# Kernel tuning notes

Measured on AMD Instinct MI355X. Metric: run time of the kernel, lower is better.

## Reference

```python
import jax, jax.numpy as jnp
import numpy as np

B, S, D_MODEL = 2, 2048, 768
N_QK, D_QK = 16, 16
N_OV, D_OV = 256, 1
VKV = 16
ROT_DIM, ROT_BASE = 16, 10000.0
SCALE = D_QK ** 0.5  # attn_scale defaults to sqrt(d_qk_head)


def _rotary_sin_cos(n_ctx, rotary_dim, base):
    # TransformerLens-style, non-adjacent pairs (GPT-NeoX)
    pos = jnp.arange(n_ctx, dtype=jnp.float32)
    dim = jnp.arange(rotary_dim // 2, dtype=jnp.float32)
    freq = base ** (dim / (rotary_dim / 2))
    freq = jnp.concatenate([freq, freq])  # 'd -> (2 d)'
    angles = pos[:, None] / freq[None, :]  # [n_ctx, rotary_dim]
    return jnp.sin(angles), jnp.cos(angles)


def _apply_rotary(x, sin, cos):
    # x: [B, S, H, d_head]; rotate first ROT_DIM dims, pass through the rest
    s = x.shape[1]
    xr = x[..., :ROT_DIM]
    half = ROT_DIM // 2
    rot = jnp.concatenate([-xr[..., half:], xr[..., :half]], axis=-1)  # rotate_every_two (non-adjacent)
    xr = xr * cos[:s, None, :] + rot * sin[:s, None, :]
    return jnp.concatenate([xr, x[..., ROT_DIM:]], axis=-1) if x.shape[-1] > ROT_DIM else xr


def setup_inputs() -> dict:
    key = jax.random.key(0)
    ks = jax.random.split(key, 6)
    std_qk = np.sqrt(2.0 / (D_MODEL * D_QK))   # kaiming fan_in for [H, d_model, d_head]
    std_v = np.sqrt(2.0 / (D_MODEL * D_OV))
    std_o = np.sqrt(2.0 / (D_OV * D_MODEL))
    std_vk = np.sqrt(2.0 / (N_QK * D_QK))
    return {
        "resid": jax.random.normal(ks[0], (B, S, D_MODEL), jnp.float32),
        "W_Q": jax.random.normal(ks[1], (N_QK, D_MODEL, D_QK), jnp.float32) * std_qk,
        "W_K": jax.random.normal(ks[2], (N_QK, D_MODEL, D_QK), jnp.float32) * std_qk,
        "W_V": jax.random.normal(ks[3], (N_OV, D_MODEL, D_OV), jnp.float32) * std_v,
        "W_O": jax.random.normal(ks[4], (N_OV, D_OV, D_MODEL), jnp.float32) * std_o,
        "b_Q": jnp.zeros((N_QK, D_QK), jnp.float32),
        "b_K": jnp.zeros((N_QK, D_QK), jnp.float32),
        "b_V": jnp.zeros((N_OV, D_OV), jnp.float32),
        "b_O": jnp.zeros((D_MODEL,), jnp.float32),
        "virtual_k": jax.random.normal(ks[5], (VKV, N_QK, D_QK), jnp.float32) * std_vk,
        "virtual_v": jnp.zeros((VKV, N_OV, D_OV), jnp.float32),
    }


def reference(resid, W_Q, W_K, W_V, W_O, b_Q, b_K, b_V, b_O, virtual_k, virtual_v):
    b, s, _ = resid.shape
    sin, cos = _rotary_sin_cos(s, ROT_DIM, ROT_BASE)

    q = jnp.einsum('bsd,hde->bshe', resid, W_Q) + b_Q  # [B,S,N_QK,D_QK]
    k = jnp.einsum('bsd,hde->bshe', resid, W_K) + b_K
    v = jnp.einsum('bsd,hde->bshe', resid, W_V) + b_V  # [B,S,N_OV,1]

    q = _apply_rotary(q, sin, cos)
    k = _apply_rotary(k, sin, cos)

    # append virtual KV along key axis
    k = jnp.concatenate([k, jnp.broadcast_to(virtual_k[None], (b, VKV, N_QK, D_QK))], axis=1)
    v = jnp.concatenate([v, jnp.broadcast_to(virtual_v[None], (b, VKV, N_OV, D_OV))], axis=1)

    scores = jnp.einsum('bqhe,bkhe->bhqk', q, k) / SCALE  # [B,H,S,S+VKV]
    i = jnp.arange(s)[:, None]
    j = jnp.arange(s + VKV)[None, :]
    mask = (j - i) <= VKV  # tril(.., diagonal=VKV)
    scores = jnp.where(mask, scores, -jnp.inf)
    pattern = jax.nn.softmax(scores, axis=-1)
    pattern = jnp.where(jnp.isnan(pattern), 0.0, pattern)

    r = N_OV // N_QK
    v_r = v.transpose(0, 2, 1, 3).reshape(b, N_QK, r, s + VKV, D_OV)  # [B,n_qk,r,K,1]
    z = jnp.einsum('bnqk,bnrkh->bnrqh', pattern, v_r)  # [B,n_qk,r,S,1]
    z = z.reshape(b, N_OV, s, D_OV).transpose(0, 2, 1, 3)  # [B,S,N_OV,1]

    out = jnp.einsum('bqhd,hdm->bqm', z, W_O) + b_O  # [B,S,D_MODEL]
    return out
```

## Files before the change

### kernel.cpp

```cpp
#include <hip/hip_runtime.h>
#include <hip/hip_bf16.h>
#include <math.h>

#define B_   2
#define S_   2048
#define DM   768
#define H_   16
#define C_   256
#define VKV_ 16
#define SK   2064
#define SKP  2080
#define NT_  65

#define TSPLIT 16
#define MAXSP  5
#define NACT   164

typedef __attribute__((ext_vector_type(8))) short short8;
typedef __attribute__((ext_vector_type(4))) short short4v;
typedef __attribute__((ext_vector_type(4))) float f32x4;
typedef __attribute__((ext_vector_type(16))) float f32x16;
typedef __attribute__((ext_vector_type(4))) unsigned uint4v;

#define QSCALE 0.360673760222240851f
#define L2B8   1.6609640474436811f

__device__ __forceinline__ short tobf(float f) {
    union { float f; unsigned u; } x; x.f = f;
    unsigned r = x.u + 0x7FFFu + ((x.u >> 16) & 1u);
    return (short)(r >> 16);
}
__device__ __forceinline__ float frombf_lo(unsigned u) {
    union { unsigned u; float f; } x; x.u = u << 16; return x.f;
}
__device__ __forceinline__ float frombf_hi(unsigned u) {
    union { unsigned u; float f; } x; x.u = u & 0xFFFF0000u; return x.f;
}

__device__ __forceinline__ void gload_lds16(const short* g, short* l) {
    __builtin_amdgcn_global_load_lds(
        (const __attribute__((address_space(1))) unsigned int*)g,
        (__attribute__((address_space(3))) unsigned int*)l, 16, 0, 0);
}

#define NRES (4096*768/4)
#define NWQ  (768*768)
#define NWO  (768*256)
__global__ __launch_bounds__(256) void conv_all(
    const float* __restrict__ resid,
    const float* __restrict__ WQ, const float* __restrict__ WK,
    const float* __restrict__ WV, const float* __restrict__ WO,
    const float* __restrict__ bQ, const float* __restrict__ bK,
    const float* __restrict__ bV,
    const float* __restrict__ vKp, const float* __restrict__ vVp,
    short* __restrict__ Ab, short* __restrict__ Wqkv_t,
    short* __restrict__ WtO, float* __restrict__ bqkv,
    short* __restrict__ Kb2, short* __restrict__ Vt3)
{
    int t = blockIdx.x * 256 + threadIdx.x;
    if (t < NRES) {
        float4 v = *(const float4*)(resid + (size_t)t * 4);
        short4v o = { tobf(v.x), tobf(v.y), tobf(v.z), tobf(v.w) };
        *(short4v*)(Ab + (size_t)t * 4) = o;
        return;
    }
    t -= NRES;
    if (t < NWQ) {
        int cc = t / 768, d = t % 768;
        float w;
        if (cc < 256)      w = WQ[((size_t)(cc >> 4) * DM + d) * 16 + (cc & 15)];
        else if (cc < 512) w = WK[((size_t)((cc - 256) >> 4) * DM + d) * 16 + (cc & 15)];
        else               w = WV[(size_t)(cc - 512) * DM + d];
        Wqkv_t[t] = tobf(w);
        return;
    }
    t -= NWQ;
    if (t < NWO) {
        int c = t & 255, m = t >> 8;
        WtO[t] = tobf(WO[(size_t)c * DM + m]);
        return;
    }
    t -= NWO;
    if (t < 768) {
        bqkv[t] = (t < 256) ? bQ[t] : (t < 512 ? bK[t - 256] : bV[t - 512]);
        return;
    }
    t -= 768;
    if (t < 32 * 32) {
        const int bh = t >> 5;
        const int s  = S_ + (t & 31);
        const int h  = bh & 15;
        short kb[16], vb[16];
        if (s < SK) {
            const int tt = s - S_;
#pragma unroll
            for (int e = 0; e < 16; ++e) {
                kb[e] = tobf(vKp[(size_t)tt * 256 + h * 16 + e]);
                vb[e] = tobf(vVp[(size_t)tt * 256 + h * 16 + e]);
            }
        } else {
#pragma unroll
            for (int e = 0; e < 16; ++e) { kb[e] = 0; vb[e] = 0; }
        }
        const int t5 = s >> 5;
        short* kbase = Kb2 + ((size_t)bh * NT_ + t5) * 512 + (s & 31) * 8;
#pragma unroll
        for (int e = 0; e < 8; ++e)  { kbase[e] = kb[e]; kbase[256 + e] = kb[e + 8]; }
        short* vbase = Vt3 + ((size_t)bh * NT_ + t5) * 1024
                     + ((s >> 4) & 1) * 512 + ((s >> 3) & 1) * 8 + (s & 7);
#pragma unroll
        for (int dv = 0; dv < 16; ++dv) vbase[dv * 16] = vb[dv];
    }
}

__global__ __launch_bounds__(256) void mm_qkv(
    const short* __restrict__ A, const short* __restrict__ Bt,
    const float* __restrict__ bias,
    short* __restrict__ Qb2, short* __restrict__ Kb2, short* __restrict__ Vt3)
{
    __shared__ short As[128 * 64];
    __shared__ short Bs[64 * 64];

    const int tid  = threadIdx.x;
    const int w    = tid >> 6;
    const int lane = tid & 63;
    const int wm   = w >> 1, wn = w & 1;
    const int g    = lane >> 4, c = lane & 15;

    const int linear = blockIdx.y * 12 + blockIdx.x;
    const int xcd  = linear & 7;
    const int jj2  = linear >> 3;
    const int m0   = (xcd * 4 + jj2 / 12) * 128;
    const int n0   = (jj2 % 12) * 64;

    f32x4 acc[4][2];
#pragma unroll
    for (int i = 0; i < 4; ++i)
#pragma unroll
        for (int j = 0; j < 2; ++j) acc[i][j] = (f32x4){0.f, 0.f, 0.f, 0.f};

    const int lr = lane >> 3;
    const int lc = lane & 7;

    for (int k0 = 0; k0 < 768; k0 += 64) {
#pragma unroll
        for (int i = 0; i < 4; ++i) {
            const int ch  = i * 4 + w;
            const int row = ch * 8 + lr;
            const int scc = lc ^ (row & 7);
            gload_lds16(A + (size_t)(m0 + row) * 768 + k0 + scc * 8, As + ch * 512);
        }
#pragma unroll
        for (int i = 0; i < 2; ++i) {
            const int ch  = i * 4 + w;
            const int row = ch * 8 + lr;
            const int scc = lc ^ (row & 7);
            gload_lds16(Bt + (size_t)(n0 + row) * 768 + k0 + scc * 8, Bs + ch * 512);
        }
        __syncthreads();
#pragma unroll
        for (int kk = 0; kk < 64; kk += 32) {
            short8 af[4], bf[2];
#pragma unroll
            for (int i = 0; i < 4; ++i) {
                const int row = wm * 64 + i * 16 + c;
                const int sc  = ((kk >> 3) + g) ^ (row & 7);
                af[i] = *(const short8*)(As + row * 64 + sc * 8);
            }
#pragma unroll
            for (int j = 0; j < 2; ++j) {
                const int row = wn * 32 + j * 16 + c;
                const int sc  = ((kk >> 3) + g) ^ (row & 7);
                bf[j] = *(const short8*)(Bs + row * 64 + sc * 8);
            }
#pragma unroll
            for (int i = 0; i < 4; ++i)
#pragma unroll
                for (int j = 0; j < 2; ++j)
                    acc[i][j] = __builtin_amdgcn_mfma_f32_16x16x32_bf16(
                        af[i], bf[j], acc[i][j], 0, 0, 0);
        }
        __syncthreads();
    }

    const float bv0 = bias[n0 + wn * 32 + c];
    const float bv1 = bias[n0 + wn * 32 + 16 + c];

    if (n0 < 512) {
        const int isQ = (n0 < 256) ? 1 : 0;
        const float invf = __builtin_amdgcn_exp2f(-(float)(c & 7) * L2B8);
        const int h0 = (((n0 + wn * 32) & 255) >> 4);
        const int elo = (c & 8) ? 0 : 1;
#pragma unroll
        for (int i = 0; i < 4; ++i) {
#pragma unroll
            for (int r = 0; r < 4; ++r) {
                const int row = m0 + wm * 64 + i * 16 + 4 * g + r;
                const int s   = row & 2047;
                const int b   = row >> 11;
                float sn, cs;
                __sincosf((float)s * invf, &sn, &cs);
#pragma unroll
                for (int j = 0; j < 2; ++j) {
                    float val = acc[i][j][r] + (j ? bv1 : bv0);
                    float par = __shfl_xor(val, 8);
                    float rot = elo ? -par : par;
                    float out = val * cs + rot * sn;
                    if (isQ) out *= QSCALE;
                    const int bh = b * 16 + h0 + j;
                    const size_t base = isQ
                        ? ((size_t)bh * 64 + (s >> 5)) * 512
                        : ((size_t)bh * NT_ + (s >> 5)) * 512;
                    short* dst = (isQ ? Qb2 : Kb2) + base
                               + (s & 31) * 8 + (c >> 3) * 256 + (c & 7);
                    *dst = tobf(out);
                }
            }
        }
    } else {
        const int h0 = ((n0 + wn * 32 - 512) >> 4);
#pragma unroll
        for (int i = 0; i < 4; ++i) {
#pragma unroll
            for (int r = 0; r < 4; ++r) {
                const int row = m0 + wm * 64 + i * 16 + 4 * g + r;
                const int s   = row & 2047;
                const int b   = row >> 11;
#pragma unroll
                for (int j = 0; j < 2; ++j) {
                    float val = acc[i][j][r] + (j ? bv1 : bv0);
                    const int bh = b * 16 + h0 + j;
                    short* dst = Vt3 + ((size_t)bh * NT_ + (s >> 5)) * 1024
                               + ((s >> 4) & 1) * 512 + ((s >> 3) & 1) * 8 + (s & 7)
                               + c * 16;
                    *dst = tobf(val);
                }
            }
        }
    }
}

__global__ __launch_bounds__(256) void mm_out(
    const short* __restrict__ A, const short* __restrict__ Bt,
    const float* __restrict__ bias, float* __restrict__ Cout)
{
    __shared__ short As[128 * 64];
    __shared__ short Bs[64 * 64];

    const int tid  = threadIdx.x;
    const int w    = tid >> 6;
    const int lane = tid & 63;
    const int wm   = w >> 1, wn = w & 1;
    const int g    = lane >> 4, c = lane & 15;

    const int linear = blockIdx.y * 12 + blockIdx.x;
    const int xcd  = linear & 7;
    const int jj2  = linear >> 3;
    const int m0   = (xcd * 4 + jj2 / 12) * 128;
    const int n0   = (jj2 % 12) * 64;

    f32x4 acc[4][2];
#pragma unroll
    for (int i = 0; i < 4; ++i)
#pragma unroll
        for (int j = 0; j < 2; ++j) acc[i][j] = (f32x4){0.f, 0.f, 0.f, 0.f};

    const int lr = lane >> 3;
    const int lc = lane & 7;

    for (int k0 = 0; k0 < 256; k0 += 64) {
#pragma unroll
        for (int i = 0; i < 4; ++i) {
            const int ch  = i * 4 + w;
            const int row = ch * 8 + lr;
            const int scc = lc ^ (row & 7);
            gload_lds16(A + (size_t)(m0 + row) * 256 + k0 + scc * 8, As + ch * 512);
        }
#pragma unroll
        for (int i = 0; i < 2; ++i) {
            const int ch  = i * 4 + w;
            const int row = ch * 8 + lr;
            const int scc = lc ^ (row & 7);
            gload_lds16(Bt + (size_t)(n0 + row) * 256 + k0 + scc * 8, Bs + ch * 512);
        }
        __syncthreads();
#pragma unroll
        for (int kk = 0; kk < 64; kk += 32) {
            short8 af[4], bf[2];
#pragma unroll
            for (int i = 0; i < 4; ++i) {
                const int row = wm * 64 + i * 16 + c;
                const int sc  = ((kk >> 3) + g) ^ (row & 7);
                af[i] = *(const short8*)(As + row * 64 + sc * 8);
            }
#pragma unroll
            for (int j = 0; j < 2; ++j) {
                const int row = wn * 32 + j * 16 + c;
                const int sc  = ((kk >> 3) + g) ^ (row & 7);
                bf[j] = *(const short8*)(Bs + row * 64 + sc * 8);
            }
#pragma unroll
            for (int i = 0; i < 4; ++i)
#pragma unroll
                for (int j = 0; j < 2; ++j)
                    acc[i][j] = __builtin_amdgcn_mfma_f32_16x16x32_bf16(
                        af[i], bf[j], acc[i][j], 0, 0, 0);
        }
        __syncthreads();
    }
#pragma unroll
    for (int i = 0; i < 4; ++i)
#pragma unroll
        for (int j = 0; j < 2; ++j) {
            const int col = n0 + wn * 32 + j * 16 + c;
            const float bv = bias[col];
#pragma unroll
            for (int r = 0; r < 4; ++r) {
                const int row = m0 + wm * 64 + i * 16 + 4 * g + r;
                Cout[(size_t)row * DM + col] = acc[i][j][r] + bv;
            }
        }
}

__global__ __launch_bounds__(256) void attn_split(
    const short* __restrict__ Qb2, const short* __restrict__ Kb2,
    const short* __restrict__ Vt3, unsigned* __restrict__ PartA,
    float* __restrict__ PartL)
{
    const int w    = threadIdx.x >> 6;
    const int lane = threadIdx.x & 63;
    const int blk  = blockIdx.x;
    const int xcd  = blk & 7;
    const int j    = blk >> 3;
    const int bhl  = j / 41;
    const int slot = j - bhl * 41;
    const int bh   = xcd * 4 + bhl;
    const int r    = slot * 4 + w;
    int qt, sp;
    if (r < 49)       { sp = 1; qt = 15 + r; }
    else if (r < 82)  { sp = 2; qt = 31 + (r - 49); }
    else if (r < 99)  { sp = 3; qt = 47 + (r - 82); }
    else if (r == 99) { sp = 4; qt = 63; }
    else              { sp = 0; qt = 163 - r; }

    const int nt   = qt + 2;
    const int t0   = sp * TSPLIT;
    const int tend = min(t0 + TSPLIT, nt);

    const int hi = lane >> 5;
    const int qc = lane & 31;
    const int q0 = qt * 32;

    const f32x16 zero16 = {0,0,0,0,0,0,0,0,0,0,0,0,0,0,0,0};

    short8 qf = *(const short8*)(Qb2 + ((size_t)bh * 64 + qt) * 512 + lane * 8);

    f32x16 acc = zero16;
    float lsum = 0.f;

    const short* kbase = Kb2 + (size_t)bh * NT_ * 512 + lane * 8;
    const short* vbase = Vt3 + (size_t)bh * NT_ * 1024 + (lane & 15) * 16 + hi * 8;
    const int qv16  = q0 + qc + 16;
    const int tmask = (q0 + 17) >> 5;

#define LK(tt)  (*(const short8*)(kbase + (size_t)(tt) * 512))
#define LVA(tt) (*(const short8*)(vbase + (size_t)(tt) * 1024))
#define LVB(tt) (*(const short8*)(vbase + (size_t)(tt) * 1024 + 512))

#define SOFTMAX_TILE(S, tt, B1, B2)                                          \
    {                                                                        \
        if ((tt) >= tmask) {                                                 \
            const int kt_ = (tt) * 32;                                       \
            _Pragma("unroll")                                                \
            for (int rr = 0; rr < 16; ++rr) {                                \
                const int key = kt_ + (rr & 3) + 8 * (rr >> 2) + 4 * hi;     \
                S[rr] = (key <= qv16) ? S[rr] : -INFINITY;                   \
            }                                                                \
        }                                                                    \
        unsigned pk[8];                                                      \
        _Pragma("unroll")                                                    \
        for (int jj = 0; jj < 8; ++jj) {                                     \
            const float p0 = __builtin_amdgcn_exp2f(S[2 * jj]);              \
            const float p1 = __builtin_amdgcn_exp2f(S[2 * jj + 1]);          \
            lsum += p0 + p1;                                                 \
            asm("v_cvt_pk_bf16_f32 %0, %1, %2" : "=v"(pk[jj]) : "v"(p0), "v"(p1)); \
        }                                                                    \
        unsigned a0 = pk[0], a2 = pk[2], a1 = pk[1], a3 = pk[3];             \
        unsigned a4 = pk[4], a6 = pk[6], a5 = pk[5], a7 = pk[7];             \
        asm("v_permlane32_swap_b32 %0, %1" : "+v"(a0), "+v"(a2));            \
        asm("v_permlane32_swap_b32 %0, %1" : "+v"(a1), "+v"(a3));            \
        asm("v_permlane32_swap_b32 %0, %1" : "+v"(a4), "+v"(a6));            \
        asm("v_permlane32_swap_b32 %0, %1" : "+v"(a5), "+v"(a7));            \
        B1.u[0] = a0; B1.u[1] = a1; B1.u[2] = a2; B1.u[3] = a3;              \
        B2.u[0] = a4; B2.u[1] = a5; B2.u[2] = a6; B2.u[3] = a7;              \
    }

    const int npair_end = t0 + ((tend - t0) & ~1);

    if (t0 < npair_end) {
        short8 kfA = LK(t0),     vaA = LVA(t0),     vvA = LVB(t0);
        short8 kfB = LK(t0 + 1), vaB = LVA(t0 + 1), vvB = LVB(t0 + 1);

        for (int t = t0; t < npair_end; t += 2) {
            short8 kfA_n = kfA, vaA_n = vaA, vvA_n = vvA;
            short8 kfB_n = kfB, vaB_n = vaB, vvB_n = vvB;
            if (t + 2 < npair_end) {
                kfA_n = LK(t + 2); vaA_n = LVA(t + 2); vvA_n = LVB(t + 2);
                kfB_n = LK(t + 3); vaB_n = LVA(t + 3); vvB_n = LVB(t + 3);
            }

            __builtin_amdgcn_s_setprio(1);
            f32x16 S0 = __builtin_amdgcn_mfma_f32_32x32x16_bf16(kfA, qf, zero16, 0, 0, 0);
            f32x16 S1 = __builtin_amdgcn_mfma_f32_32x32x16_bf16(kfB, qf, zero16, 0, 0, 0);
            __builtin_amdgcn_s_setprio(0);

            union { unsigned u[4]; short8 v; } b1A, b2A, b1B, b2B;
            SOFTMAX_TILE(S0, t,     b1A, b2A);
            SOFTMAX_TILE(S1, t + 1, b1B, b2B);

            __builtin_amdgcn_s_setprio(1);
            acc = __builtin_amdgcn_mfma_f32_32x32x16_bf16(vaA, b1A.v, acc, 0, 0, 0);
            acc = __builtin_amdgcn_mfma_f32_32x32x16_bf16(vvA, b2A.v, acc, 0, 0, 0);
            acc = __builtin_amdgcn_mfma_f32_32x32x16_bf16(vaB, b1B.v, acc, 0, 0, 0);
            acc = __builtin_amdgcn_mfma_f32_32x32x16_bf16(vvB, b2B.v, acc, 0, 0, 0);
            __builtin_amdgcn_s_setprio(0);

            kfA = kfA_n; vaA = vaA_n; vvA = vvA_n;
            kfB = kfB_n; vaB = vaB_n; vvB = vvB_n;
        }
    }
    if (npair_end < tend) {
        const int t = npair_end;
        short8 kf = LK(t), va = LVA(t), vv = LVB(t);
        f32x16 S0 = __builtin_amdgcn_mfma_f32_32x32x16_bf16(kf, qf, zero16, 0, 0, 0);
        union { unsigned u[4]; short8 v; } b1, b2;
        SOFTMAX_TILE(S0, t, b1, b2);
        acc = __builtin_amdgcn_mfma_f32_32x32x16_bf16(va, b1.v, acc, 0, 0, 0);
        acc = __builtin_amdgcn_mfma_f32_32x32x16_bf16(vv, b2.v, acc, 0, 0, 0);
    }

    uint4v pa;
    asm("v_cvt_pk_bf16_f32 %0, %1, %2" : "=v"(pa.x) : "v"(acc[0]), "v"(acc[1]));
    asm("v_cvt_pk_bf16_f32 %0, %1, %2" : "=v"(pa.y) : "v"(acc[2]), "v"(acc[3]));
    asm("v_cvt_pk_bf16_f32 %0, %1, %2" : "=v"(pa.z) : "v"(acc[4]), "v"(acc[5]));
    asm("v_cvt_pk_bf16_f32 %0, %1, %2" : "=v"(pa.w) : "v"(acc[6]), "v"(acc[7]));

    const int pidx = (bh * 64 + qt) * MAXSP + sp;
    *(uint4v*)(PartA + ((size_t)pidx * 64 + lane) * 4) = pa;

    lsum += __shfl_xor(lsum, 32);
    if (hi == 0) PartL[(size_t)pidx * 32 + qc] = lsum;
}

__global__ __launch_bounds__(256) void attn_combine(
    const unsigned* __restrict__ PartA, const float* __restrict__ PartL,
    short* __restrict__ Zb)
{
    const int w    = threadIdx.x >> 6;
    const int lane = threadIdx.x & 63;
    const int wid  = blockIdx.x * 4 + w;
    const int bh   = wid >> 6;
    const int qt   = wid & 63;
    const int hi   = lane >> 5;
    const int qc   = lane & 31;
    const int ns   = (qt + 2 + TSPLIT - 1) / TSPLIT;

    float a[8];
#pragma unroll
    for (int rr = 0; rr < 8; ++rr) a[rr] = 0.f;
    float lsum = 0.f;

    const int pbase = (bh * 64 + qt) * MAXSP;
    for (int sp = 0; sp < ns; ++sp) {
        uint4v pa = *(const uint4v*)(PartA + ((size_t)(pbase + sp) * 64 + lane) * 4);
        a[0] += frombf_lo(pa.x); a[1] += frombf_hi(pa.x);
        a[2] += frombf_lo(pa.y); a[3] += frombf_hi(pa.y);
        a[4] += frombf_lo(pa.z); a[5] += frombf_hi(pa.z);
        a[6] += frombf_lo(pa.w); a[7] += frombf_hi(pa.w);
        lsum += PartL[(size_t)(pbase + sp) * 32 + qc];
    }
    const float inv = 1.f / lsum;

    const int b = bh >> 4, h = bh & 15;
    const int q0 = qt * 32;
    short* zp = Zb + ((size_t)(b * S_ + q0 + qc)) * C_ + h * 16;
    unsigned o01, o23, o45, o67;
    {
        float a0 = a[0] * inv, a1 = a[1] * inv, a2 = a[2] * inv, a3 = a[3] * inv;
        float a4 = a[4] * inv, a5 = a[5] * inv, a6 = a[6] * inv, a7 = a[7] * inv;
        asm("v_cvt_pk_bf16_f32 %0, %1, %2" : "=v"(o01) : "v"(a0), "v"(a1));
        asm("v_cvt_pk_bf16_f32 %0, %1, %2" : "=v"(o23) : "v"(a2), "v"(a3));
        asm("v_cvt_pk_bf16_f32 %0, %1, %2" : "=v"(o45) : "v"(a4), "v"(a5));
        asm("v_cvt_pk_bf16_f32 %0, %1, %2" : "=v"(o67) : "v"(a6), "v"(a7));
    }
    *(unsigned*)(zp + 4 * hi)         = o01;
    *(unsigned*)(zp + 4 * hi + 2)     = o23;
    *(unsigned*)(zp + 8 + 4 * hi)     = o45;
    *(unsigned*)(zp + 8 + 4 * hi + 2) = o67;
}

extern "C" void kernel_launch(void* const* d_in, const int* in_sizes, int n_in,
                              void* d_out, int out_size, void* d_ws, size_t ws_size,
                              hipStream_t stream)
{
    const float* resid = (const float*)d_in[0];
    const float* WQ = (const float*)d_in[1];
    const float* WK = (const float*)d_in[2];
    const float* WV = (const float*)d_in[3];
    const float* WO = (const float*)d_in[4];
    const float* bQ = (const float*)d_in[5];
    const float* bK = (const float*)d_in[6];
    const float* bV = (const float*)d_in[7];
    const float* bO = (const float*)d_in[8];
    const float* vK = (const float*)d_in[9];
    const float* vV = (const float*)d_in[10];
    float* out = (float*)d_out;
    float* ws  = (float*)d_ws;

    short* Zb   = (short*)ws;
    float* bqkv = ws + 3145728;
    short* Ab   = (short*)(ws + 3145728 + 768);
    short* Wqt  = Ab + 3145728;
    short* WtO  = Wqt + 589824;
    short* Qb2  = WtO + 196608;
    short* Kb2  = Qb2 + 1048576;
    short* Vt3  = Kb2 + 1064960;
    unsigned* PartA = (unsigned*)(Vt3 + 2129920);
    float*    PartL = (float*)(PartA + 2621440);

    const int conv_total = NRES + NWQ + NWO + 768 + 1024;
    conv_all<<<dim3((conv_total + 255) / 256), 256, 0, stream>>>(
        resid, WQ, WK, WV, WO, bQ, bK, bV, vK, vV,
        Ab, Wqt, WtO, bqkv, Kb2, Vt3);
    mm_qkv<<<dim3(12, 32), 256, 0, stream>>>(Ab, Wqt, bqkv, Qb2, Kb2, Vt3);
    attn_split<<<dim3(32 * NACT / 4), 256, 0, stream>>>(Qb2, Kb2, Vt3, PartA, PartL);
    attn_combine<<<dim3(512), 256, 0, stream>>>(PartA, PartL, Zb);
    mm_out<<<dim3(12, 32), 256, 0, stream>>>(Zb, WtO, bO, out);
}
```

Before: 60.02 us.

## Double-buffer LDS tiles in QKV and output GEMMs to overlap loads with MFMA

Both GEMM kernels now keep two LDS buffers for the A and B tiles. Each iteration first issues the direct-to-LDS loads for the next K tile, then runs MFMAs on the current tile, so global-memory latency can hide behind compute and one barrier per iteration goes away. In exchange, shared memory per block doubles, which may lower how many blocks fit on a CU. These GEMMs are only part of a pipeline that attention likely dominates.

```diff
diff --git a/kernel.cpp b/kernel.cpp
--- a/kernel.cpp
+++ b/kernel.cpp
@@ -118,8 +118,8 @@
     const float* __restrict__ bias,
     short* __restrict__ Qb2, short* __restrict__ Kb2, short* __restrict__ Vt3)
 {
-    __shared__ short As[128 * 64];
-    __shared__ short Bs[64 * 64];
+    __shared__ short As[2][128 * 64];
+    __shared__ short Bs[2][64 * 64];
 
     const int tid  = threadIdx.x;
     const int w    = tid >> 6;
@@ -142,22 +142,32 @@
     const int lr = lane >> 3;
     const int lc = lane & 7;
 
-    for (int k0 = 0; k0 < 768; k0 += 64) {
-#pragma unroll
-        for (int i = 0; i < 4; ++i) {
-            const int ch  = i * 4 + w;
-            const int row = ch * 8 + lr;
-            const int scc = lc ^ (row & 7);
-            gload_lds16(A + (size_t)(m0 + row) * 768 + k0 + scc * 8, As + ch * 512);
-        }
-#pragma unroll
-        for (int i = 0; i < 2; ++i) {
-            const int ch  = i * 4 + w;
-            const int row = ch * 8 + lr;
-            const int scc = lc ^ (row & 7);
-            gload_lds16(Bt + (size_t)(n0 + row) * 768 + k0 + scc * 8, Bs + ch * 512);
-        }
-        __syncthreads();
+#define MMSTAGE(k0v, buf) do {                                               \
+        _Pragma("unroll")                                                    \
+        for (int i = 0; i < 4; ++i) {                                        \
+            const int ch  = i * 4 + w;                                       \
+            const int row = ch * 8 + lr;                                     \
+            const int scc = lc ^ (row & 7);                                  \
+            gload_lds16(A + (size_t)(m0 + row) * 768 + (k0v) + scc * 8,      \
+                        &As[buf][ch * 512]);                                 \
+        }                                                                    \
+        _Pragma("unroll")                                                    \
+        for (int i = 0; i < 2; ++i) {                                        \
+            const int ch  = i * 4 + w;                                       \
+            const int row = ch * 8 + lr;                                     \
+            const int scc = lc ^ (row & 7);                                  \
+            gload_lds16(Bt + (size_t)(n0 + row) * 768 + (k0v) + scc * 8,     \
+                        &Bs[buf][ch * 512]);                                 \
+        }                                                                    \
+    } while (0)
+
+    MMSTAGE(0, 0);
+    __syncthreads();
+
+    for (int kt = 0; kt < 12; ++kt) {
+        if (kt + 1 < 12) MMSTAGE((kt + 1) * 64, (kt + 1) & 1);
+        const short* Ab_ = &As[kt & 1][0];
+        const short* Bb_ = &Bs[kt & 1][0];
 #pragma unroll
         for (int kk = 0; kk < 64; kk += 32) {
             short8 af[4], bf[2];
@@ -165,13 +175,13 @@
             for (int i = 0; i < 4; ++i) {
                 const int row = wm * 64 + i * 16 + c;
                 const int sc  = ((kk >> 3) + g) ^ (row & 7);
-                af[i] = *(const short8*)(As + row * 64 + sc * 8);
+                af[i] = *(const short8*)(Ab_ + row * 64 + sc * 8);
             }
 #pragma unroll
             for (int j = 0; j < 2; ++j) {
                 const int row = wn * 32 + j * 16 + c;
                 const int sc  = ((kk >> 3) + g) ^ (row & 7);
-                bf[j] = *(const short8*)(Bs + row * 64 + sc * 8);
+                bf[j] = *(const short8*)(Bb_ + row * 64 + sc * 8);
             }
 #pragma unroll
             for (int i = 0; i < 4; ++i)
@@ -182,6 +192,7 @@
         }
         __syncthreads();
     }
+#undef MMSTAGE
 
     const float bv0 = bias[n0 + wn * 32 + c];
     const float bv1 = bias[n0 + wn * 32 + 16 + c];
@@ -244,8 +255,8 @@
     const short* __restrict__ A, const short* __restrict__ Bt,
     const float* __restrict__ bias, float* __restrict__ Cout)
 {
-    __shared__ short As[128 * 64];
-    __shared__ short Bs[64 * 64];
+    __shared__ short As[2][128 * 64];
+    __shared__ short Bs[2][64 * 64];
 
     const int tid  = threadIdx.x;
     const int w    = tid >> 6;
@@ -268,22 +279,32 @@
     const int lr = lane >> 3;
     const int lc = lane & 7;
 
-    for (int k0 = 0; k0 < 256; k0 += 64) {
-#pragma unroll
-        for (int i = 0; i < 4; ++i) {
-            const int ch  = i * 4 + w;
-            const int row = ch * 8 + lr;
-            const int scc = lc ^ (row & 7);
-            gload_lds16(A + (size_t)(m0 + row) * 256 + k0 + scc * 8, As + ch * 512);
-        }
-#pragma unroll
-        for (int i = 0; i < 2; ++i) {
-            const int ch  = i * 4 + w;
-            const int row = ch * 8 + lr;
-            const int scc = lc ^ (row & 7);
-            gload_lds16(Bt + (size_t)(n0 + row) * 256 + k0 + scc * 8, Bs + ch * 512);
-        }
-        __syncthreads();
+#define MMSTAGE2(k0v, buf) do {                                              \
+        _Pragma("unroll")                                                    \
+        for (int i = 0; i < 4; ++i) {                                        \
+            const int ch  = i * 4 + w;                                       \
+            const int row = ch * 8 + lr;                                     \
+            const int scc = lc ^ (row & 7);                                  \
+            gload_lds16(A + (size_t)(m0 + row) * 256 + (k0v) + scc * 8,      \
+                        &As[buf][ch * 512]);                                 \
+        }                                                                    \
+        _Pragma("unroll")                                                    \
+        for (int i = 0; i < 2; ++i) {                                        \
+            const int ch  = i * 4 + w;                                       \
+            const int row = ch * 8 + lr;                                     \
+            const int scc = lc ^ (row & 7);                                  \
+            gload_lds16(Bt + (size_t)(n0 + row) * 256 + (k0v) + scc * 8,     \
+                        &Bs[buf][ch * 512]);                                 \
+        }                                                                    \
+    } while (0)
+
+    MMSTAGE2(0, 0);
+    __syncthreads();
+
+    for (int kt = 0; kt < 4; ++kt) {
+        if (kt + 1 < 4) MMSTAGE2((kt + 1) * 64, (kt + 1) & 1);
+        const short* Ab_ = &As[kt & 1][0];
+        const short* Bb_ = &Bs[kt & 1][0];
 #pragma unroll
         for (int kk = 0; kk < 64; kk += 32) {
             short8 af[4], bf[2];
@@ -291,13 +312,13 @@
             for (int i = 0; i < 4; ++i) {
                 const int row = wm * 64 + i * 16 + c;
                 const int sc  = ((kk >> 3) + g) ^ (row & 7);
-                af[i] = *(const short8*)(As + row * 64 + sc * 8);
+                af[i] = *(const short8*)(Ab_ + row * 64 + sc * 8);
             }
 #pragma unroll
             for (int j = 0; j < 2; ++j) {
                 const int row = wn * 32 + j * 16 + c;
                 const int sc  = ((kk >> 3) + g) ^ (row & 7);
-                bf[j] = *(const short8*)(Bs + row * 64 + sc * 8);
+                bf[j] = *(const short8*)(Bb_ + row * 64 + sc * 8);
             }
 #pragma unroll
             for (int i = 0; i < 4; ++i)
@@ -308,6 +329,8 @@
         }
         __syncthreads();
     }
+#undef MMSTAGE2
+
 #pragma unroll
     for (int i = 0; i < 4; ++i)
 #pragma unroll
```

New measurement: 61.44 us. 1.02x slower.

## Stage QKV GEMM epilogue through LDS for vectorized rotary and V stores

Applied to the files above, without the earlier changes.

The QKV GEMM epilogue now writes accumulators to a padded LDS tile, reusing the A/B staging memory, then has each thread rebuild whole 16-element head rows. This lets it apply rotary without cross-lane shuffles and emit 16-byte vector stores instead of scattered 2-byte stores. The weight-prep kernel also changes its thread-to-element mapping so Q/K weight reads are coalesced. The cost is an extra LDS round trip and a barrier, plus a larger shared allocation that may reduce occupancy.

```diff
diff --git a/kernel.cpp b/kernel.cpp
--- a/kernel.cpp
+++ b/kernel.cpp
@@ -66,12 +66,18 @@
     }
     t -= NRES;
     if (t < NWQ) {
-        int cc = t / 768, d = t % 768;
+        int cc, d;
+        if (t < 512 * 768) {
+            const int e    = t & 15;
+            const int rest = t >> 4;
+            d  = rest % 768;
+            cc = (rest / 768) * 16 + e;
+        } else { cc = t / 768; d = t % 768; }
         float w;
         if (cc < 256)      w = WQ[((size_t)(cc >> 4) * DM + d) * 16 + (cc & 15)];
         else if (cc < 512) w = WK[((size_t)((cc - 256) >> 4) * DM + d) * 16 + (cc & 15)];
         else               w = WV[(size_t)(cc - 512) * DM + d];
-        Wqkv_t[t] = tobf(w);
+        Wqkv_t[(size_t)cc * 768 + d] = tobf(w);
         return;
     }
     t -= NWQ;
@@ -118,8 +124,9 @@
     const float* __restrict__ bias,
     short* __restrict__ Qb2, short* __restrict__ Kb2, short* __restrict__ Vt3)
 {
-    __shared__ short As[128 * 64];
-    __shared__ short Bs[64 * 64];
+    __shared__ float CtS[128][65];
+    short* As = (short*)&CtS[0][0];
+    short* Bs = (short*)&CtS[0][0] + 8192;
 
     const int tid  = threadIdx.x;
     const int w    = tid >> 6;
@@ -183,59 +190,65 @@
         __syncthreads();
     }
 
-    const float bv0 = bias[n0 + wn * 32 + c];
-    const float bv1 = bias[n0 + wn * 32 + 16 + c];
-
+#pragma unroll
+    for (int i = 0; i < 4; ++i)
+#pragma unroll
+        for (int j = 0; j < 2; ++j)
+#pragma unroll
+            for (int r = 0; r < 4; ++r)
+                CtS[wm * 64 + i * 16 + 4 * g + r][wn * 32 + j * 16 + c] = acc[i][j][r];
+    __syncthreads();
+
+    const int b = m0 >> 11;
     if (n0 < 512) {
-        const int isQ = (n0 < 256) ? 1 : 0;
-        const float invf = __builtin_amdgcn_exp2f(-(float)(c & 7) * L2B8);
-        const int h0 = (((n0 + wn * 32) & 255) >> 4);
-        const int elo = (c & 8) ? 0 : 1;
-#pragma unroll
-        for (int i = 0; i < 4; ++i) {
-#pragma unroll
-            for (int r = 0; r < 4; ++r) {
-                const int row = m0 + wm * 64 + i * 16 + 4 * g + r;
-                const int s   = row & 2047;
-                const int b   = row >> 11;
+        const int isQ   = n0 < 256;
+        const int hbase = (n0 & 255) >> 4;
+#pragma unroll
+        for (int it = 0; it < 2; ++it) {
+            const int idx  = it * 256 + tid;
+            const int srow = idx & 127;
+            const int g16  = idx >> 7;
+            const int s    = (m0 + srow) & 2047;
+            const int bh   = b * 16 + hbase + g16;
+            float v[16];
+#pragma unroll
+            for (int e = 0; e < 16; ++e)
+                v[e] = CtS[srow][g16 * 16 + e] + bias[n0 + g16 * 16 + e];
+            union { short s[16]; short8 v8[2]; } u;
+#pragma unroll
+            for (int e = 0; e < 8; ++e) {
+                const float invf = __builtin_amdgcn_exp2f(-(float)e * L2B8);
                 float sn, cs;
                 __sincosf((float)s * invf, &sn, &cs);
-#pragma unroll
-                for (int j = 0; j < 2; ++j) {
-                    float val = acc[i][j][r] + (j ? bv1 : bv0);
-                    float par = __shfl_xor(val, 8);
-                    float rot = elo ? -par : par;
-                    float out = val * cs + rot * sn;
-                    if (isQ) out *= QSCALE;
-                    const int bh = b * 16 + h0 + j;
-                    const size_t base = isQ
-                        ? ((size_t)bh * 64 + (s >> 5)) * 512
-                        : ((size_t)bh * NT_ + (s >> 5)) * 512;
-                    short* dst = (isQ ? Qb2 : Kb2) + base
-                               + (s & 31) * 8 + (c >> 3) * 256 + (c & 7);
-                    *dst = tobf(out);
-                }
-            }
+                float o0 = v[e] * cs - v[e + 8] * sn;
+                float o1 = v[e + 8] * cs + v[e] * sn;
+                if (isQ) { o0 *= QSCALE; o1 *= QSCALE; }
+                u.s[e] = tobf(o0); u.s[e + 8] = tobf(o1);
+            }
+            short* dst = (isQ ? Qb2 + ((size_t)bh * 64 + (s >> 5)) * 512
+                              : Kb2 + ((size_t)bh * NT_ + (s >> 5)) * 512)
+                       + (s & 31) * 8;
+            *(short8*)dst         = u.v8[0];
+            *(short8*)(dst + 256) = u.v8[1];
         }
     } else {
-        const int h0 = ((n0 + wn * 32 - 512) >> 4);
-#pragma unroll
-        for (int i = 0; i < 4; ++i) {
-#pragma unroll
-            for (int r = 0; r < 4; ++r) {
-                const int row = m0 + wm * 64 + i * 16 + 4 * g + r;
-                const int s   = row & 2047;
-                const int b   = row >> 11;
-#pragma unroll
-                for (int j = 0; j < 2; ++j) {
-                    float val = acc[i][j][r] + (j ? bv1 : bv0);
-                    const int bh = b * 16 + h0 + j;
-                    short* dst = Vt3 + ((size_t)bh * NT_ + (s >> 5)) * 1024
-                               + ((s >> 4) & 1) * 512 + ((s >> 3) & 1) * 8 + (s & 7)
-                               + c * 16;
-                    *dst = tobf(val);
-                }
-            }
+        const int hbase = (n0 - 512) >> 4;
+#pragma unroll
+        for (int it = 0; it < 2; ++it) {
+            const int idx = it * 256 + tid;
+            const int dvl = idx & 63;
+            const int rg  = idx >> 6;
+            const int s0  = (m0 + rg * 16) & 2047;
+            const int bh  = b * 16 + hbase + (dvl >> 4);
+            const float bv = bias[n0 + dvl];
+            union { short s[16]; short8 v8[2]; } u;
+#pragma unroll
+            for (int k = 0; k < 16; ++k)
+                u.s[k] = tobf(CtS[rg * 16 + k][dvl] + bv);
+            short* dst = Vt3 + ((size_t)bh * NT_ + (s0 >> 5)) * 1024
+                       + ((s0 >> 4) & 1) * 512 + (dvl & 15) * 16;
+            *(short8*)dst       = u.v8[0];
+            *(short8*)(dst + 8) = u.v8[1];
         }
     }
 }
```

Measured after the change: 58.21 us. 3.0% less time.
